# Performance work log

Measured on AMD Instinct MI355X. Metric: run time of the kernel, lower is better.

The kernel has to match this reference:

```python
import jax, jax.numpy as jnp
import numpy as np

T, B, N, E, NF, L = 4, 8, 5000, 80000, 16, 3


def setup_inputs() -> dict:
    key = jax.random.key(0)
    ks = jax.random.split(key, 12)
    xs = jax.random.normal(ks[0], (T, B, N, 3), jnp.float32)
    vs = jax.random.normal(ks[1], (T, B, N, 3), jnp.float32)
    charges = jax.random.uniform(ks[2], (B * N, 1), jnp.float32)
    edge_src = jax.random.randint(ks[3], (E,), 0, N)
    edge_dst = jax.random.randint(ks[4], (E,), 0, N)
    theta = jax.random.uniform(ks[5], (1, T), jnp.float32, -1.0, 1.0)  # uniform_(-1,1)
    W_embed = jax.random.normal(ks[6], (1, NF), jnp.float32) * 0.5
    W1 = jax.random.normal(ks[7], (L, 2 * NF + 1, NF), jnp.float32) / jnp.sqrt(2.0 * NF + 1)
    b1 = jnp.zeros((L, NF), jnp.float32)
    W2 = jax.random.normal(ks[8], (L, NF, NF), jnp.float32) / jnp.sqrt(float(NF))
    b2 = jnp.zeros((L, NF), jnp.float32)
    Wv = jax.random.normal(ks[9], (L, NF, 1), jnp.float32) * 0.1
    return dict(xs=xs, vs=vs, charges=charges, edge_src=edge_src, edge_dst=edge_dst,
                theta=theta, W_embed=W_embed, W1=W1, b1=b1, W2=W2, b2=b2, Wv=Wv)


def reference(xs, vs, charges, edge_src, edge_dst, theta, W_embed, W1, b1, W2, b2, Wv):
    T_, B_, N_, _ = xs.shape
    # node scalar features ('f' / type-0) initialized from charges
    h0 = jax.nn.relu(charges.reshape(B_, N_, 1) @ W_embed)  # [B, N, NF]

    def graph_step(x, v, h):
        # x, v: [N,3]; h: [N,NF]. Equivariant message passing with edge rel-pos gather.
        d = x[edge_dst] - x[edge_src]                      # [E,3]  (edata['d'])
        d2 = jnp.sum(d * d, axis=-1, keepdims=True)        # [E,1]  invariant edge feature
        vec = v                                            # type-1 ('vel') channel
        for l in range(L):
            feat = jnp.concatenate([h[edge_src], h[edge_dst], d2], axis=-1)  # [E,2NF+1]
            m = jax.nn.relu(feat @ W1[l] + b1[l])                            # [E,NF]
            agg = jax.ops.segment_sum(m, edge_dst, num_segments=N_)          # [N,NF]
            h = h + jax.nn.relu(agg @ W2[l] + b2[l])
            # equivariant vector update: scatter d-weighted messages
            vec = vec + jax.ops.segment_sum(d * (m @ Wv[l]), edge_dst, num_segments=N_)
        return vec + x  # module returns out + xs

    step_b = jax.vmap(graph_step)                                  # over batch
    out = jax.vmap(lambda x, v: step_b(x, v, h0))(xs, vs)          # [T,B,N,3]
    x = out.reshape(T_, B_ * N_, 3)                                # step's view(-1, 3)
    x_hat = jnp.einsum('ij,jkt->ikt', jax.nn.softmax(theta, axis=1), x)
    return x_hat.squeeze(0)  # [B*N, 3] since num_future == 1
```

## Files before the change

kernel.cpp:

```cpp
#include <hip/hip_runtime.h>
#include <hip/hip_bf16.h>

constexpr int T_ = 4;
constexpr int B_ = 8;
constexpr int N_ = 5000;
constexpr int E_ = 80000;
constexpr int TBN = T_ * B_ * N_;
constexpr int NXCD = 8;

constexpr int NPB = 64;
constexpr int CH  = (N_ + NPB - 1) / NPB;
constexpr int GRP = T_ * B_ / NXCD;
constexpr int LB  = NXCD * CH * GRP;

__device__ __forceinline__ unsigned bf16pack2(float lo, float hi) {
    unsigned ul = (__float_as_uint(lo) + 0x8000u) >> 16;
    unsigned uh = (__float_as_uint(hi) + 0x8000u) & 0xffff0000u;
    return uh | ul;
}
__device__ __forceinline__ void bf16unpack2(unsigned u, float& lo, float& hi) {
    lo = __uint_as_float(u << 16);
    hi = __uint_as_float(u & 0xffff0000u);
}

__global__ void k_degree(const int* __restrict__ dst, int* __restrict__ deg) {
    int e = blockIdx.x * 256 + threadIdx.x;
    if (e < E_) atomicAdd(&deg[dst[e]], 1);
}

__global__ void k_scan(const int* __restrict__ deg, int* __restrict__ row_start) {
    __shared__ int sums[256];
    const int tid = threadIdx.x;
    const int per = 20;
    const int base = tid * per;
    int local = 0;
    for (int i = 0; i < per; ++i) {
        int idx = base + i;
        if (idx < N_) local += deg[idx];
    }
    sums[tid] = local;
    __syncthreads();
    for (int off = 1; off < 256; off <<= 1) {
        int v = 0;
        if (tid >= off) v = sums[tid - off];
        __syncthreads();
        if (tid >= off) sums[tid] += v;
        __syncthreads();
    }
    int running = sums[tid] - local;
    for (int i = 0; i < per; ++i) {
        int idx = base + i;
        if (idx < N_) {
            row_start[idx] = running;
            running += deg[idx];
        }
    }
    if (tid == 255) row_start[N_] = sums[255];
}

__global__ void k_scatter(const int* __restrict__ src, const int* __restrict__ dst,
                          const int* __restrict__ row_start, int* __restrict__ cursor,
                          int* __restrict__ csr_src) {
    int e = blockIdx.x * 256 + threadIdx.x;
    if (e < E_) {
        int d = dst[e];
        int pos = atomicAdd(&cursor[d], 1);
        csr_src[row_start[d] + pos] = src[e];
    }
}

__global__ void k_init(const float* __restrict__ xs, float4* __restrict__ xs4) {
    int g = blockIdx.x * 256 + threadIdx.x;
    xs4[g] = make_float4(xs[3*g], xs[3*g+1], xs[3*g+2], 0.0f);
}

template <int LYR, bool HAS_NEXT>
__global__ __launch_bounds__(256, 4) void k_layer(
        const float4* __restrict__ xs4, const float* __restrict__ charges,
        const float* __restrict__ vs, const float* __restrict__ W_embed,
        const float* __restrict__ W1, const float* __restrict__ b1,
        const float* __restrict__ W2, const float* __restrict__ b2,
        const float* __restrict__ Wv,
        const int* __restrict__ row_start, const int* __restrict__ csr_src,
        float* __restrict__ h, const uint4* __restrict__ gs_in,
        uint2* __restrict__ gs_out, unsigned* __restrict__ gd,
        float* __restrict__ vec) {
    __shared__ float s_w1e[16], s_wv[16], s_b2[16], s_b1[16], s_b1n[16];
    __shared__ float s_W2[256];
    __shared__ float s_W1sn[256];
    __shared__ float s_W1dn[256];
    __shared__ float s_P[16], s_Q[16], s_rwe[16];
    const int tid = threadIdx.x;
    if (tid < 16) {
        s_w1e[tid] = W1[LYR * 528 + 512 + tid];
        s_wv[tid]  = Wv[LYR * 16 + tid];
        s_b2[tid]  = b2[LYR * 16 + tid];
        s_b1[tid]  = b1[LYR * 16 + tid];
        if (HAS_NEXT) s_b1n[tid] = b1[(LYR + 1) * 16 + tid];
    }
    s_W2[tid] = W2[LYR * 256 + tid];
    if (HAS_NEXT) {
        s_W1sn[tid] = W1[(LYR + 1) * 528 + tid];
        s_W1dn[tid] = W1[(LYR + 1) * 528 + 256 + tid];
    }
    if (LYR == 0 && tid < 16) {
        float accP = 0.0f, accQ = 0.0f;
        for (int j = 0; j < 16; ++j) {
            float r = fmaxf(W_embed[j], 0.0f);
            accP += r * W1[j * 16 + tid];
            accQ += r * W1[256 + j * 16 + tid];
        }
        s_P[tid] = accP; s_Q[tid] = accQ;
        s_rwe[tid] = fmaxf(W_embed[tid], 0.0f);
    }
    __syncthreads();

    const int bid   = blockIdx.x;
    const int xcd   = bid & 7;
    const int j     = bid >> 3;
    const int tb    = xcd + NXCD * (j / CH);
    const int chunk = j % CH;
    const int node  = chunk * NPB + (tid >> 2);
    const int q     = tid & 3;
    if (node >= N_) return;

    const int g = tb * N_ + node;
    const size_t nb = (size_t)tb * N_;
    const float* cb = charges + (tb % B_) * N_;

    const float4 xn = xs4[g];

    float gdn[16];
    float c0 = 0.0f;
    if (LYR == 0) {
        c0 = cb[node];
#pragma unroll
        for (int f = 0; f < 16; ++f) gdn[f] = c0 * s_Q[f] + s_b1[f];
    } else {
        const uint4* gdp = (const uint4*)gd + (size_t)g * 2;
        uint4 da = gdp[0], db = gdp[1];
        bf16unpack2(da.x, gdn[0], gdn[1]);  bf16unpack2(da.y, gdn[2], gdn[3]);
        bf16unpack2(da.z, gdn[4], gdn[5]);  bf16unpack2(da.w, gdn[6], gdn[7]);
        bf16unpack2(db.x, gdn[8], gdn[9]);  bf16unpack2(db.y, gdn[10], gdn[11]);
        bf16unpack2(db.z, gdn[12], gdn[13]); bf16unpack2(db.w, gdn[14], gdn[15]);
    }

    float agg[16];
#pragma unroll
    for (int f = 0; f < 16; ++f) agg[f] = 0.0f;
    float av0 = 0.0f, av1 = 0.0f, av2 = 0.0f;

    const int rs = row_start[node];
    const int re = row_start[node + 1];

    int e = rs + q;
    bool have = e < re;
    int s = have ? csr_src[e] : 0;
    size_t si = nb + (size_t)s;
    float4 xc = xs4[si];
    float  cs = 0.0f;
    uint4  ga, gb;
    if (LYR == 0) cs = cb[s];
    else { ga = gs_in[si * 2]; gb = gs_in[si * 2 + 1]; }

    while (have) {
        int e2 = e + 4;
        bool have2 = e2 < re;
        int s2 = have2 ? csr_src[e2] : 0;
        size_t si2 = nb + (size_t)s2;
        float4 xc2 = xs4[si2];
        float  cs2 = 0.0f;
        uint4  ga2, gb2;
        if (LYR == 0) cs2 = cb[s2];
        else { ga2 = gs_in[si2 * 2]; gb2 = gs_in[si2 * 2 + 1]; }

        float d0 = xn.x - xc.x;
        float d1 = xn.y - xc.y;
        float d2v = xn.z - xc.z;
        float dd = d0*d0 + d1*d1 + d2v*d2v;

        float gsf[16];
        if (LYR == 0) {
#pragma unroll
            for (int f = 0; f < 16; ++f) gsf[f] = cs * s_P[f];
        } else {
            bf16unpack2(ga.x, gsf[0], gsf[1]);  bf16unpack2(ga.y, gsf[2], gsf[3]);
            bf16unpack2(ga.z, gsf[4], gsf[5]);  bf16unpack2(ga.w, gsf[6], gsf[7]);
            bf16unpack2(gb.x, gsf[8], gsf[9]);  bf16unpack2(gb.y, gsf[10], gsf[11]);
            bf16unpack2(gb.z, gsf[12], gsf[13]); bf16unpack2(gb.w, gsf[14], gsf[15]);
        }

        float sval = 0.0f;
#pragma unroll
        for (int f = 0; f < 16; ++f) {
            float mv = fmaxf(__builtin_fmaf(dd, s_w1e[f], gdn[f]) + gsf[f], 0.0f);
            if (HAS_NEXT) agg[f] += mv;
            sval = __builtin_fmaf(mv, s_wv[f], sval);
        }
        av0 = __builtin_fmaf(d0, sval, av0);
        av1 = __builtin_fmaf(d1, sval, av1);
        av2 = __builtin_fmaf(d2v, sval, av2);

        e = e2; have = have2; xc = xc2; cs = cs2; ga = ga2; gb = gb2;
    }

    av0 += __shfl_xor(av0, 1); av0 += __shfl_xor(av0, 2);
    av1 += __shfl_xor(av1, 1); av1 += __shfl_xor(av1, 2);
    av2 += __shfl_xor(av2, 1); av2 += __shfl_xor(av2, 2);

    if (q < 3) {
        float myav = (q == 0) ? av0 : ((q == 1) ? av1 : av2);
        size_t vi = (size_t)g * 3 + q;
        float base = (LYR == 0) ? vs[vi] : vec[vi];
        vec[vi] = base + myav;
    }

    if (HAS_NEXT) {
#pragma unroll
        for (int f = 0; f < 16; ++f) {
            agg[f] += __shfl_xor(agg[f], 1);
            agg[f] += __shfl_xor(agg[f], 2);
        }

        float hq[4];
        if (LYR == 0) {
#pragma unroll
            for (int k = 0; k < 4; ++k) hq[k] = c0 * s_rwe[q * 4 + k];
        } else {
            float4 hv = ((const float4*)h)[(size_t)g * 4 + q];
            hq[0] = hv.x; hq[1] = hv.y; hq[2] = hv.z; hq[3] = hv.w;
        }

        float acc[4];
#pragma unroll
        for (int k = 0; k < 4; ++k) acc[k] = s_b2[q * 4 + k];
#pragma unroll
        for (int jj = 0; jj < 16; ++jj) {
            float aj = agg[jj];
#pragma unroll
            for (int k = 0; k < 4; ++k)
                acc[k] = __builtin_fmaf(aj, s_W2[jj * 16 + q * 4 + k], acc[k]);
        }
#pragma unroll
        for (int k = 0; k < 4; ++k) hq[k] += fmaxf(acc[k], 0.0f);

        const int lane = tid & 63;
        const int lbase = lane & ~3;
        float hfull[16];
#pragma unroll
        for (int sq = 0; sq < 4; ++sq) {
#pragma unroll
            for (int k = 0; k < 4; ++k)
                hfull[sq * 4 + k] = __shfl(hq[k], lbase + sq, 64);
        }

        float gso[4], gdo[4];
#pragma unroll
        for (int k = 0; k < 4; ++k) { gso[k] = 0.0f; gdo[k] = s_b1n[q * 4 + k]; }
#pragma unroll
        for (int jj = 0; jj < 16; ++jj) {
            float hj = hfull[jj];
#pragma unroll
            for (int k = 0; k < 4; ++k) {
                gso[k] = __builtin_fmaf(hj, s_W1sn[jj * 16 + q * 4 + k], gso[k]);
                gdo[k] = __builtin_fmaf(hj, s_W1dn[jj * 16 + q * 4 + k], gdo[k]);
            }
        }

        ((float4*)h)[(size_t)g * 4 + q] = make_float4(hq[0], hq[1], hq[2], hq[3]);
        gs_out[(size_t)g * 4 + q] = make_uint2(bf16pack2(gso[0], gso[1]),
                                               bf16pack2(gso[2], gso[3]));
        ((uint2*)gd)[(size_t)g * 4 + q] = make_uint2(bf16pack2(gdo[0], gdo[1]),
                                                     bf16pack2(gdo[2], gdo[3]));
    }
}

__global__ void k_final(const float* __restrict__ xs, const float* __restrict__ vec,
                        const float* __restrict__ theta, float* __restrict__ out) {
    int g = blockIdx.x * 256 + threadIdx.x;
    if (g >= B_ * N_) return;
    float t0 = theta[0], t1 = theta[1], t2 = theta[2], t3 = theta[3];
    float mx = fmaxf(fmaxf(t0, t1), fmaxf(t2, t3));
    float e0 = expf(t0 - mx), e1 = expf(t1 - mx), e2 = expf(t2 - mx), e3 = expf(t3 - mx);
    float inv = 1.0f / (e0 + e1 + e2 + e3);
    float w[4] = {e0 * inv, e1 * inv, e2 * inv, e3 * inv};

    int b = g / N_;
    int n = g - b * N_;
    float o0 = 0.0f, o1 = 0.0f, o2 = 0.0f;
#pragma unroll
    for (int t = 0; t < 4; ++t) {
        size_t idx = ((size_t)(t * B_ + b) * N_ + n) * 3;
        o0 += w[t] * (vec[idx+0] + xs[idx+0]);
        o1 += w[t] * (vec[idx+1] + xs[idx+1]);
        o2 += w[t] * (vec[idx+2] + xs[idx+2]);
    }
    out[(size_t)g*3+0] = o0;
    out[(size_t)g*3+1] = o1;
    out[(size_t)g*3+2] = o2;
}

extern "C" void kernel_launch(void* const* d_in, const int* in_sizes, int n_in,
                              void* d_out, int out_size, void* d_ws, size_t ws_size,
                              hipStream_t stream) {
    const float* xs       = (const float*)d_in[0];
    const float* vs       = (const float*)d_in[1];
    const float* charges  = (const float*)d_in[2];
    const int*   edge_src = (const int*)d_in[3];
    const int*   edge_dst = (const int*)d_in[4];
    const float* theta    = (const float*)d_in[5];
    const float* W_embed  = (const float*)d_in[6];
    const float* W1       = (const float*)d_in[7];
    const float* b1       = (const float*)d_in[8];
    const float* W2       = (const float*)d_in[9];
    const float* b2       = (const float*)d_in[10];
    const float* Wv       = (const float*)d_in[11];
    float* out = (float*)d_out;

    char* w = (char*)d_ws;
    size_t off = 0;
    auto take = [&](size_t bytes) {
        size_t o = off;
        off = (off + bytes + 255) & ~(size_t)255;
        return o;
    };
    int*      deg       = (int*)(w + take((size_t)N_ * 4));
    int*      cursor    = (int*)(w + take((size_t)N_ * 4));
    int*      row_start = (int*)(w + take((size_t)(N_ + 1) * 4));
    int*      csr_src   = (int*)(w + take((size_t)E_ * 4));
    float*    h         = (float*)(w + take((size_t)TBN * 16 * 4));
    unsigned* gsA       = (unsigned*)(w + take((size_t)TBN * 32));
    unsigned* gsB       = (unsigned*)(w + take((size_t)TBN * 32));
    unsigned* gd        = (unsigned*)(w + take((size_t)TBN * 32));
    float*    vec       = (float*)(w + take((size_t)TBN * 3 * 4));
    float4*   xs4       = (float4*)(w + take((size_t)TBN * 16));
    (void)ws_size;

    hipMemsetAsync(deg, 0, (size_t)N_ * 4, stream);
    hipMemsetAsync(cursor, 0, (size_t)N_ * 4, stream);

    const int eb = (E_ + 255) / 256;
    k_degree<<<eb, 256, 0, stream>>>(edge_dst, deg);
    k_scan<<<1, 256, 0, stream>>>(deg, row_start);
    k_scatter<<<eb, 256, 0, stream>>>(edge_src, edge_dst, row_start, cursor, csr_src);

    k_init<<<TBN / 256, 256, 0, stream>>>(xs, xs4);

    k_layer<0, true ><<<LB, 256, 0, stream>>>(xs4, charges, vs, W_embed, W1, b1, W2, b2, Wv,
                                              row_start, csr_src, h, nullptr,
                                              (uint2*)gsA, gd, vec);
    k_layer<1, true ><<<LB, 256, 0, stream>>>(xs4, charges, vs, W_embed, W1, b1, W2, b2, Wv,
                                              row_start, csr_src, h, (const uint4*)gsA,
                                              (uint2*)gsB, gd, vec);
    k_layer<2, false><<<LB, 256, 0, stream>>>(xs4, charges, vs, W_embed, W1, b1, W2, b2, Wv,
                                              row_start, csr_src, h, (const uint4*)gsB,
                                              nullptr, gd, vec);

    const int fb = (B_ * N_ + 255) / 256;
    k_final<<<fb, 256, 0, stream>>>(xs, vec, theta, out);
}
```

Baseline: 124.6 us.

## Sort nodes by in-degree for balanced wavefronts and deepen CSR prefetch

Adds a single-block counting sort that builds a permutation of nodes ordered by in-degree, and the layer kernels map threads to nodes through it. Nodes of similar degree then share a wavefront, which cuts divergence from uneven edge loops. The edge loop now prefetches the source index two steps ahead using clamped loads, and the two memsets are merged into one. Costs are an extra kernel launch, an indirection through perm, and scattered writes to per-node outputs.

```diff
diff --git a/kernel.cpp b/kernel.cpp
--- a/kernel.cpp
+++ b/kernel.cpp
@@ -69,6 +69,31 @@
     }
 }
 
+__global__ void k_perm(const int* __restrict__ deg, int* __restrict__ perm) {
+    __shared__ int hist[64];
+    __shared__ int base[64];
+    const int tid = threadIdx.x;
+    if (tid < 64) hist[tid] = 0;
+    __syncthreads();
+    for (int idx = tid; idx < N_; idx += 256) {
+        int d = min(deg[idx], 63);
+        atomicAdd(&hist[d], 1);
+    }
+    __syncthreads();
+    if (tid == 0) {
+        int running = 0;
+        for (int b = 0; b < 64; ++b) { base[b] = running; running += hist[b]; }
+    }
+    __syncthreads();
+    if (tid < 64) hist[tid] = 0;
+    __syncthreads();
+    for (int idx = tid; idx < N_; idx += 256) {
+        int d = min(deg[idx], 63);
+        int pos = atomicAdd(&hist[d], 1);
+        perm[base[d] + pos] = idx;
+    }
+}
+
 __global__ void k_init(const float* __restrict__ xs, float4* __restrict__ xs4) {
     int g = blockIdx.x * 256 + threadIdx.x;
     xs4[g] = make_float4(xs[3*g], xs[3*g+1], xs[3*g+2], 0.0f);
@@ -82,6 +107,7 @@
         const float* __restrict__ W2, const float* __restrict__ b2,
         const float* __restrict__ Wv,
         const int* __restrict__ row_start, const int* __restrict__ csr_src,
+        const int* __restrict__ perm,
         float* __restrict__ h, const uint4* __restrict__ gs_in,
         uint2* __restrict__ gs_out, unsigned* __restrict__ gd,
         float* __restrict__ vec) {
@@ -120,9 +146,10 @@
     const int j     = bid >> 3;
     const int tb    = xcd + NXCD * (j / CH);
     const int chunk = j % CH;
-    const int node  = chunk * NPB + (tid >> 2);
+    const int idx   = chunk * NPB + (tid >> 2);
     const int q     = tid & 3;
-    if (node >= N_) return;
+    if (idx >= N_) return;
+    const int node  = perm[idx];
 
     const int g = tb * N_ + node;
     const size_t nb = (size_t)tb * N_;
@@ -154,25 +181,23 @@
     const int re = row_start[node + 1];
 
     int e = rs + q;
-    bool have = e < re;
-    int s = have ? csr_src[e] : 0;
-    size_t si = nb + (size_t)s;
+    int sCur  = csr_src[min(e, E_ - 1)];
+    int sNext = csr_src[min(e + 4, E_ - 1)];
+    size_t si = nb + (size_t)sCur;
     float4 xc = xs4[si];
     float  cs = 0.0f;
     uint4  ga, gb;
-    if (LYR == 0) cs = cb[s];
+    if (LYR == 0) cs = cb[sCur];
     else { ga = gs_in[si * 2]; gb = gs_in[si * 2 + 1]; }
 
-    while (have) {
-        int e2 = e + 4;
-        bool have2 = e2 < re;
-        int s2 = have2 ? csr_src[e2] : 0;
-        size_t si2 = nb + (size_t)s2;
-        float4 xc2 = xs4[si2];
-        float  cs2 = 0.0f;
-        uint4  ga2, gb2;
-        if (LYR == 0) cs2 = cb[s2];
-        else { ga2 = gs_in[si2 * 2]; gb2 = gs_in[si2 * 2 + 1]; }
+    while (e < re) {
+        int s3 = csr_src[min(e + 8, E_ - 1)];
+        size_t siN = nb + (size_t)sNext;
+        float4 xcN = xs4[siN];
+        float  csN = 0.0f;
+        uint4  gaN, gbN;
+        if (LYR == 0) csN = cb[sNext];
+        else { gaN = gs_in[siN * 2]; gbN = gs_in[siN * 2 + 1]; }
 
         float d0 = xn.x - xc.x;
         float d1 = xn.y - xc.y;
@@ -201,7 +226,9 @@
         av1 = __builtin_fmaf(d1, sval, av1);
         av2 = __builtin_fmaf(d2v, sval, av2);
 
-        e = e2; have = have2; xc = xc2; cs = cs2; ga = ga2; gb = gb2;
+        e += 4;
+        sNext = s3;
+        xc = xcN; cs = csN; ga = gaN; gb = gbN;
     }
 
     av0 += __shfl_xor(av0, 1); av0 += __shfl_xor(av0, 2);
@@ -328,6 +355,7 @@
     int*      cursor    = (int*)(w + take((size_t)N_ * 4));
     int*      row_start = (int*)(w + take((size_t)(N_ + 1) * 4));
     int*      csr_src   = (int*)(w + take((size_t)E_ * 4));
+    int*      perm      = (int*)(w + take((size_t)N_ * 4));
     float*    h         = (float*)(w + take((size_t)TBN * 16 * 4));
     unsigned* gsA       = (unsigned*)(w + take((size_t)TBN * 32));
     unsigned* gsB       = (unsigned*)(w + take((size_t)TBN * 32));
@@ -336,24 +364,25 @@
     float4*   xs4       = (float4*)(w + take((size_t)TBN * 16));
     (void)ws_size;
 
-    hipMemsetAsync(deg, 0, (size_t)N_ * 4, stream);
-    hipMemsetAsync(cursor, 0, (size_t)N_ * 4, stream);
+    size_t zlen = (size_t)((char*)cursor - (char*)deg) + (size_t)N_ * 4;
+    hipMemsetAsync(deg, 0, zlen, stream);
 
     const int eb = (E_ + 255) / 256;
     k_degree<<<eb, 256, 0, stream>>>(edge_dst, deg);
     k_scan<<<1, 256, 0, stream>>>(deg, row_start);
+    k_perm<<<1, 256, 0, stream>>>(deg, perm);
     k_scatter<<<eb, 256, 0, stream>>>(edge_src, edge_dst, row_start, cursor, csr_src);
 
     k_init<<<TBN / 256, 256, 0, stream>>>(xs, xs4);
 
     k_layer<0, true ><<<LB, 256, 0, stream>>>(xs4, charges, vs, W_embed, W1, b1, W2, b2, Wv,
-                                              row_start, csr_src, h, nullptr,
+                                              row_start, csr_src, perm, h, nullptr,
                                               (uint2*)gsA, gd, vec);
     k_layer<1, true ><<<LB, 256, 0, stream>>>(xs4, charges, vs, W_embed, W1, b1, W2, b2, Wv,
-                                              row_start, csr_src, h, (const uint4*)gsA,
+                                              row_start, csr_src, perm, h, (const uint4*)gsA,
                                               (uint2*)gsB, gd, vec);
     k_layer<2, false><<<LB, 256, 0, stream>>>(xs4, charges, vs, W_embed, W1, b1, W2, b2, Wv,
-                                              row_start, csr_src, h, (const uint4*)gsB,
+                                              row_start, csr_src, perm, h, (const uint4*)gsB,
                                               nullptr, gd, vec);
 
     const int fb = (B_ * N_ + 255) / 256;
```

Result: slower. 136.9 us (+9.9%).

## Sort nodes by in-degree into permuted slots and fuse CSR build

Applied to the files above, without the earlier changes.

Nodes are relabelled by a counting sort on in-degree, so the four lanes per node in a block handle neighbours of similar degree and divergence in the edge loop drops. All per-node arrays (positions, velocities, charges, features) are stored in permuted slot order, and the CSR source indices are translated to slots. The degree count, scan and permutation build are merged into one single-block shared-memory kernel, which replaces the memsets and two small launches. The cost is an extra perm lookup per node, a gather in init and final, and a serial single-block build that could become a bottleneck.

```diff
diff --git a/kernel.cpp b/kernel.cpp
--- a/kernel.cpp
+++ b/kernel.cpp
@@ -23,65 +23,95 @@
     hi = __uint_as_float(u & 0xffff0000u);
 }
 
-__global__ void k_degree(const int* __restrict__ dst, int* __restrict__ deg) {
-    int e = blockIdx.x * 256 + threadIdx.x;
-    if (e < E_) atomicAdd(&deg[dst[e]], 1);
-}
-
-__global__ void k_scan(const int* __restrict__ deg, int* __restrict__ row_start) {
-    __shared__ int sums[256];
+__global__ __launch_bounds__(1024) void k_build1(
+        const int* __restrict__ edge_dst, int* __restrict__ row_start,
+        int* __restrict__ perm, int* __restrict__ inv, int* __restrict__ cursor) {
+    __shared__ int sdeg[5120];
+    __shared__ int ssum[1024];
+    __shared__ int hist[64];
+    __shared__ int hbase[64];
     const int tid = threadIdx.x;
-    const int per = 20;
-    const int base = tid * per;
-    int local = 0;
-    for (int i = 0; i < per; ++i) {
-        int idx = base + i;
-        if (idx < N_) local += deg[idx];
-    }
-    sums[tid] = local;
-    __syncthreads();
-    for (int off = 1; off < 256; off <<= 1) {
+    for (int i = tid; i < 5120; i += 1024) sdeg[i] = 0;
+    __syncthreads();
+    for (int e = tid; e < E_; e += 1024) atomicAdd(&sdeg[edge_dst[e]], 1);
+    __syncthreads();
+    const int base = tid * 5;
+    int loc = 0;
+#pragma unroll
+    for (int i = 0; i < 5; ++i) { int ix = base + i; if (ix < N_) loc += sdeg[ix]; }
+    ssum[tid] = loc;
+    __syncthreads();
+    for (int off = 1; off < 1024; off <<= 1) {
         int v = 0;
-        if (tid >= off) v = sums[tid - off];
+        if (tid >= off) v = ssum[tid - off];
         __syncthreads();
-        if (tid >= off) sums[tid] += v;
+        if (tid >= off) ssum[tid] += v;
         __syncthreads();
     }
-    int running = sums[tid] - local;
-    for (int i = 0; i < per; ++i) {
-        int idx = base + i;
-        if (idx < N_) {
-            row_start[idx] = running;
-            running += deg[idx];
-        }
-    }
-    if (tid == 255) row_start[N_] = sums[255];
-}
-
-__global__ void k_scatter(const int* __restrict__ src, const int* __restrict__ dst,
-                          const int* __restrict__ row_start, int* __restrict__ cursor,
-                          int* __restrict__ csr_src) {
+    int run = ssum[tid] - loc;
+#pragma unroll
+    for (int i = 0; i < 5; ++i) {
+        int ix = base + i;
+        if (ix < N_) { row_start[ix] = run; run += sdeg[ix]; }
+    }
+    if (tid == 1023) row_start[N_] = ssum[1023];
+    for (int i = tid; i < N_; i += 1024) cursor[i] = 0;
+    if (tid < 64) hist[tid] = 0;
+    __syncthreads();
+    for (int i = tid; i < N_; i += 1024) atomicAdd(&hist[min(sdeg[i], 63)], 1);
+    __syncthreads();
+    if (tid == 0) {
+        int r = 0;
+        for (int b = 0; b < 64; ++b) { hbase[b] = r; r += hist[b]; }
+    }
+    __syncthreads();
+    if (tid < 64) hist[tid] = 0;
+    __syncthreads();
+    for (int i = tid; i < N_; i += 1024) {
+        int d = min(sdeg[i], 63);
+        int p = atomicAdd(&hist[d], 1);
+        int slot = hbase[d] + p;
+        perm[slot] = i;
+        inv[i] = slot;
+    }
+}
+
+__global__ void k_build2(const int* __restrict__ src, const int* __restrict__ dst,
+                         const int* __restrict__ row_start, int* __restrict__ cursor,
+                         const int* __restrict__ inv, int* __restrict__ csr_srcT) {
     int e = blockIdx.x * 256 + threadIdx.x;
     if (e < E_) {
         int d = dst[e];
         int pos = atomicAdd(&cursor[d], 1);
-        csr_src[row_start[d] + pos] = src[e];
-    }
-}
-
-__global__ void k_init(const float* __restrict__ xs, float4* __restrict__ xs4) {
+        csr_srcT[row_start[d] + pos] = inv[src[e]];
+    }
+}
+
+__global__ void k_init(const float* __restrict__ xs, const float* __restrict__ vs,
+                       const float* __restrict__ charges, const int* __restrict__ perm,
+                       float4* __restrict__ xs4, float* __restrict__ vec,
+                       float* __restrict__ chs) {
     int g = blockIdx.x * 256 + threadIdx.x;
-    xs4[g] = make_float4(xs[3*g], xs[3*g+1], xs[3*g+2], 0.0f);
+    int tb = g / N_;
+    int i  = g - tb * N_;
+    int node = perm[i];
+    size_t sn = (size_t)tb * N_ + node;
+    xs4[g] = make_float4(xs[3*sn], xs[3*sn+1], xs[3*sn+2], 0.0f);
+    vec[3*(size_t)g+0] = vs[3*sn+0];
+    vec[3*(size_t)g+1] = vs[3*sn+1];
+    vec[3*(size_t)g+2] = vs[3*sn+2];
+    if (tb < B_) chs[g] = charges[sn];
 }
 
 template <int LYR, bool HAS_NEXT>
 __global__ __launch_bounds__(256, 4) void k_layer(
-        const float4* __restrict__ xs4, const float* __restrict__ charges,
-        const float* __restrict__ vs, const float* __restrict__ W_embed,
+        const float4* __restrict__ xs4, const float* __restrict__ chs,
+        const float* __restrict__ W_embed,
         const float* __restrict__ W1, const float* __restrict__ b1,
         const float* __restrict__ W2, const float* __restrict__ b2,
         const float* __restrict__ Wv,
-        const int* __restrict__ row_start, const int* __restrict__ csr_src,
+        const int* __restrict__ row_start, const int* __restrict__ csr_srcT,
+        const int* __restrict__ perm,
         float* __restrict__ h, const uint4* __restrict__ gs_in,
         uint2* __restrict__ gs_out, unsigned* __restrict__ gd,
         float* __restrict__ vec) {
@@ -120,20 +150,20 @@
     const int j     = bid >> 3;
     const int tb    = xcd + NXCD * (j / CH);
     const int chunk = j % CH;
-    const int node  = chunk * NPB + (tid >> 2);
+    const int slot  = chunk * NPB + (tid >> 2);
     const int q     = tid & 3;
-    if (node >= N_) return;
-
-    const int g = tb * N_ + node;
+    if (slot >= N_) return;
+
+    const int g = tb * N_ + slot;
     const size_t nb = (size_t)tb * N_;
-    const float* cb = charges + (tb % B_) * N_;
+    const float* cb = chs + (tb % B_) * N_;
 
     const float4 xn = xs4[g];
 
     float gdn[16];
     float c0 = 0.0f;
     if (LYR == 0) {
-        c0 = cb[node];
+        c0 = cb[slot];
 #pragma unroll
         for (int f = 0; f < 16; ++f) gdn[f] = c0 * s_Q[f] + s_b1[f];
     } else {
@@ -150,12 +180,13 @@
     for (int f = 0; f < 16; ++f) agg[f] = 0.0f;
     float av0 = 0.0f, av1 = 0.0f, av2 = 0.0f;
 
+    const int node = perm[slot];
     const int rs = row_start[node];
     const int re = row_start[node + 1];
 
     int e = rs + q;
     bool have = e < re;
-    int s = have ? csr_src[e] : 0;
+    int s = have ? csr_srcT[e] : 0;
     size_t si = nb + (size_t)s;
     float4 xc = xs4[si];
     float  cs = 0.0f;
@@ -166,7 +197,7 @@
     while (have) {
         int e2 = e + 4;
         bool have2 = e2 < re;
-        int s2 = have2 ? csr_src[e2] : 0;
+        int s2 = have2 ? csr_srcT[e2] : 0;
         size_t si2 = nb + (size_t)s2;
         float4 xc2 = xs4[si2];
         float  cs2 = 0.0f;
@@ -211,8 +242,7 @@
     if (q < 3) {
         float myav = (q == 0) ? av0 : ((q == 1) ? av1 : av2);
         size_t vi = (size_t)g * 3 + q;
-        float base = (LYR == 0) ? vs[vi] : vec[vi];
-        vec[vi] = base + myav;
+        vec[vi] += myav;
     }
 
     if (HAS_NEXT) {
@@ -276,24 +306,27 @@
 }
 
 __global__ void k_final(const float* __restrict__ xs, const float* __restrict__ vec,
-                        const float* __restrict__ theta, float* __restrict__ out) {
+                        const float* __restrict__ theta, const int* __restrict__ inv,
+                        float* __restrict__ out) {
     int g = blockIdx.x * 256 + threadIdx.x;
     if (g >= B_ * N_) return;
     float t0 = theta[0], t1 = theta[1], t2 = theta[2], t3 = theta[3];
     float mx = fmaxf(fmaxf(t0, t1), fmaxf(t2, t3));
     float e0 = expf(t0 - mx), e1 = expf(t1 - mx), e2 = expf(t2 - mx), e3 = expf(t3 - mx);
-    float inv = 1.0f / (e0 + e1 + e2 + e3);
-    float w[4] = {e0 * inv, e1 * inv, e2 * inv, e3 * inv};
+    float is = 1.0f / (e0 + e1 + e2 + e3);
+    float w[4] = {e0 * is, e1 * is, e2 * is, e3 * is};
 
     int b = g / N_;
     int n = g - b * N_;
+    int slot = inv[n];
     float o0 = 0.0f, o1 = 0.0f, o2 = 0.0f;
 #pragma unroll
     for (int t = 0; t < 4; ++t) {
-        size_t idx = ((size_t)(t * B_ + b) * N_ + n) * 3;
-        o0 += w[t] * (vec[idx+0] + xs[idx+0]);
-        o1 += w[t] * (vec[idx+1] + xs[idx+1]);
-        o2 += w[t] * (vec[idx+2] + xs[idx+2]);
+        size_t vi = ((size_t)(t * B_ + b) * N_ + slot) * 3;
+        size_t xi = ((size_t)(t * B_ + b) * N_ + n) * 3;
+        o0 += w[t] * (vec[vi+0] + xs[xi+0]);
+        o1 += w[t] * (vec[vi+1] + xs[xi+1]);
+        o2 += w[t] * (vec[vi+2] + xs[xi+2]);
     }
     out[(size_t)g*3+0] = o0;
     out[(size_t)g*3+1] = o1;
@@ -324,38 +357,36 @@
         off = (off + bytes + 255) & ~(size_t)255;
         return o;
     };
-    int*      deg       = (int*)(w + take((size_t)N_ * 4));
     int*      cursor    = (int*)(w + take((size_t)N_ * 4));
     int*      row_start = (int*)(w + take((size_t)(N_ + 1) * 4));
-    int*      csr_src   = (int*)(w + take((size_t)E_ * 4));
+    int*      csr_srcT  = (int*)(w + take((size_t)E_ * 4));
+    int*      perm      = (int*)(w + take((size_t)N_ * 4));
+    int*      inv       = (int*)(w + take((size_t)N_ * 4));
     float*    h         = (float*)(w + take((size_t)TBN * 16 * 4));
     unsigned* gsA       = (unsigned*)(w + take((size_t)TBN * 32));
     unsigned* gsB       = (unsigned*)(w + take((size_t)TBN * 32));
     unsigned* gd        = (unsigned*)(w + take((size_t)TBN * 32));
     float*    vec       = (float*)(w + take((size_t)TBN * 3 * 4));
     float4*   xs4       = (float4*)(w + take((size_t)TBN * 16));
+    float*    chs       = (float*)(w + take((size_t)B_ * N_ * 4));
     (void)ws_size;
 
-    hipMemsetAsync(deg, 0, (size_t)N_ * 4, stream);
-    hipMemsetAsync(cursor, 0, (size_t)N_ * 4, stream);
-
+    k_build1<<<1, 1024, 0, stream>>>(edge_dst, row_start, perm, inv, cursor);
     const int eb = (E_ + 255) / 256;
-    k_degree<<<eb, 256, 0, stream>>>(edge_dst, deg);
-    k_scan<<<1, 256, 0, stream>>>(deg, row_start);
-    k_scatter<<<eb, 256, 0, stream>>>(edge_src, edge_dst, row_start, cursor, csr_src);
-
-    k_init<<<TBN / 256, 256, 0, stream>>>(xs, xs4);
-
-    k_layer<0, true ><<<LB, 256, 0, stream>>>(xs4, charges, vs, W_embed, W1, b1, W2, b2, Wv,
-                                              row_start, csr_src, h, nullptr,
+    k_build2<<<eb, 256, 0, stream>>>(edge_src, edge_dst, row_start, cursor, inv, csr_srcT);
+
+    k_init<<<TBN / 256, 256, 0, stream>>>(xs, vs, charges, perm, xs4, vec, chs);
+
+    k_layer<0, true ><<<LB, 256, 0, stream>>>(xs4, chs, W_embed, W1, b1, W2, b2, Wv,
+                                              row_start, csr_srcT, perm, h, nullptr,
                                               (uint2*)gsA, gd, vec);
-    k_layer<1, true ><<<LB, 256, 0, stream>>>(xs4, charges, vs, W_embed, W1, b1, W2, b2, Wv,
-                                              row_start, csr_src, h, (const uint4*)gsA,
+    k_layer<1, true ><<<LB, 256, 0, stream>>>(xs4, chs, W_embed, W1, b1, W2, b2, Wv,
+                                              row_start, csr_srcT, perm, h, (const uint4*)gsA,
                                               (uint2*)gsB, gd, vec);
-    k_layer<2, false><<<LB, 256, 0, stream>>>(xs4, charges, vs, W_embed, W1, b1, W2, b2, Wv,
-                                              row_start, csr_src, h, (const uint4*)gsB,
+    k_layer<2, false><<<LB, 256, 0, stream>>>(xs4, chs, W_embed, W1, b1, W2, b2, Wv,
+                                              row_start, csr_srcT, perm, h, (const uint4*)gsB,
                                               nullptr, gd, vec);
 
     const int fb = (B_ * N_ + 255) / 256;
-    k_final<<<fb, 256, 0, stream>>>(xs, vec, theta, out);
-}
+    k_final<<<fb, 256, 0, stream>>>(xs, vec, theta, inv, out);
+}
```

After: 138.8 us. +11.4%, slower.

## Pack node position, charge and source features into 64-byte records; fuse setup kernels

Applied to the files above, without the earlier changes.

Merges the degree count and scan into one single-block shared-memory kernel and fuses the CSR scatter with input packing and vec initialisation, removing two memsets and several launches. Each node's position, charge and bf16 source-side features now sit in one 64-byte record, ping-ponged between layers, so each edge gather touches one contiguous line instead of two separate arrays. The edge loop processes two edges per lane per iteration with a mask for the tail, adding memory-level parallelism. The risks are a serial single-block build kernel, wider records, and the masked second edge doing wasted work on low-degree nodes.

```diff
diff --git a/kernel.cpp b/kernel.cpp
--- a/kernel.cpp
+++ b/kernel.cpp
@@ -12,6 +12,8 @@
 constexpr int CH  = (N_ + NPB - 1) / NPB;
 constexpr int GRP = T_ * B_ / NXCD;
 constexpr int LB  = NXCD * CH * GRP;
+constexpr int EB  = (E_ + 255) / 256;
+constexpr int IB  = TBN / 256;
 
 __device__ __forceinline__ unsigned bf16pack2(float lo, float hi) {
     unsigned ul = (__float_as_uint(lo) + 0x8000u) >> 16;
@@ -23,67 +25,79 @@
     hi = __uint_as_float(u & 0xffff0000u);
 }
 
-__global__ void k_degree(const int* __restrict__ dst, int* __restrict__ deg) {
-    int e = blockIdx.x * 256 + threadIdx.x;
-    if (e < E_) atomicAdd(&deg[dst[e]], 1);
-}
-
-__global__ void k_scan(const int* __restrict__ deg, int* __restrict__ row_start) {
-    __shared__ int sums[256];
+__global__ __launch_bounds__(1024) void k_build1(
+        const int* __restrict__ edge_dst, int* __restrict__ row_start,
+        int* __restrict__ cursor) {
+    __shared__ int sdeg[5120];
+    __shared__ int ssum[1024];
     const int tid = threadIdx.x;
-    const int per = 20;
-    const int base = tid * per;
-    int local = 0;
-    for (int i = 0; i < per; ++i) {
-        int idx = base + i;
-        if (idx < N_) local += deg[idx];
-    }
-    sums[tid] = local;
+    for (int i = tid; i < 5120; i += 1024) sdeg[i] = 0;
     __syncthreads();
-    for (int off = 1; off < 256; off <<= 1) {
+    for (int e = tid; e < E_; e += 1024) atomicAdd(&sdeg[edge_dst[e]], 1);
+    __syncthreads();
+    const int base = tid * 5;
+    int loc = 0;
+#pragma unroll
+    for (int i = 0; i < 5; ++i) { int ix = base + i; if (ix < N_) loc += sdeg[ix]; }
+    ssum[tid] = loc;
+    __syncthreads();
+    for (int off = 1; off < 1024; off <<= 1) {
         int v = 0;
-        if (tid >= off) v = sums[tid - off];
+        if (tid >= off) v = ssum[tid - off];
         __syncthreads();
-        if (tid >= off) sums[tid] += v;
+        if (tid >= off) ssum[tid] += v;
         __syncthreads();
     }
-    int running = sums[tid] - local;
-    for (int i = 0; i < per; ++i) {
-        int idx = base + i;
-        if (idx < N_) {
-            row_start[idx] = running;
-            running += deg[idx];
-        }
-    }
-    if (tid == 255) row_start[N_] = sums[255];
-}
-
-__global__ void k_scatter(const int* __restrict__ src, const int* __restrict__ dst,
-                          const int* __restrict__ row_start, int* __restrict__ cursor,
-                          int* __restrict__ csr_src) {
-    int e = blockIdx.x * 256 + threadIdx.x;
-    if (e < E_) {
-        int d = dst[e];
-        int pos = atomicAdd(&cursor[d], 1);
-        csr_src[row_start[d] + pos] = src[e];
-    }
-}
-
-__global__ void k_init(const float* __restrict__ xs, float4* __restrict__ xs4) {
-    int g = blockIdx.x * 256 + threadIdx.x;
-    xs4[g] = make_float4(xs[3*g], xs[3*g+1], xs[3*g+2], 0.0f);
+    int run = ssum[tid] - loc;
+#pragma unroll
+    for (int i = 0; i < 5; ++i) {
+        int ix = base + i;
+        if (ix < N_) { row_start[ix] = run; run += sdeg[ix]; }
+    }
+    if (tid == 1023) row_start[N_] = ssum[1023];
+    for (int i = tid; i < N_; i += 1024) cursor[i] = 0;
+}
+
+__global__ void k_build2(const int* __restrict__ src, const int* __restrict__ dst,
+                         const int* __restrict__ row_start, int* __restrict__ cursor,
+                         int* __restrict__ csr_src,
+                         const float* __restrict__ xs, const float* __restrict__ vs,
+                         const float* __restrict__ charges,
+                         uint4* __restrict__ rec0, uint4* __restrict__ rec1,
+                         float* __restrict__ vec) {
+    const int bid = blockIdx.x;
+    const int tid = threadIdx.x;
+    if (bid < EB) {
+        int e = bid * 256 + tid;
+        if (e < E_) {
+            int d = dst[e];
+            int pos = atomicAdd(&cursor[d], 1);
+            csr_src[row_start[d] + pos] = src[e];
+        }
+    } else {
+        int g = (bid - EB) * 256 + tid;
+        int tb = g / N_;
+        int n  = g - tb * N_;
+        int b  = tb % B_;
+        float c = charges[b * N_ + n];
+        float4 xc = make_float4(xs[3*(size_t)g], xs[3*(size_t)g+1], xs[3*(size_t)g+2], c);
+        ((float4*)rec0)[(size_t)g * 4] = xc;
+        ((float4*)rec1)[(size_t)g * 4] = xc;
+        vec[3*(size_t)g+0] = vs[3*(size_t)g+0];
+        vec[3*(size_t)g+1] = vs[3*(size_t)g+1];
+        vec[3*(size_t)g+2] = vs[3*(size_t)g+2];
+    }
 }
 
 template <int LYR, bool HAS_NEXT>
 __global__ __launch_bounds__(256, 4) void k_layer(
-        const float4* __restrict__ xs4, const float* __restrict__ charges,
-        const float* __restrict__ vs, const float* __restrict__ W_embed,
+        const uint4* __restrict__ rec_in, uint4* __restrict__ rec_out,
+        const float* __restrict__ W_embed,
         const float* __restrict__ W1, const float* __restrict__ b1,
         const float* __restrict__ W2, const float* __restrict__ b2,
         const float* __restrict__ Wv,
         const int* __restrict__ row_start, const int* __restrict__ csr_src,
-        float* __restrict__ h, const uint4* __restrict__ gs_in,
-        uint2* __restrict__ gs_out, unsigned* __restrict__ gd,
+        float* __restrict__ h, unsigned* __restrict__ gd,
         float* __restrict__ vec) {
     __shared__ float s_w1e[16], s_wv[16], s_b2[16], s_b1[16], s_b1n[16];
     __shared__ float s_W2[256];
@@ -126,14 +140,12 @@
 
     const int g = tb * N_ + node;
     const size_t nb = (size_t)tb * N_;
-    const float* cb = charges + (tb % B_) * N_;
-
-    const float4 xn = xs4[g];
+
+    const float4 xn = ((const float4*)rec_in)[(size_t)g * 4];
+    const float c0 = xn.w;
 
     float gdn[16];
-    float c0 = 0.0f;
     if (LYR == 0) {
-        c0 = cb[node];
 #pragma unroll
         for (int f = 0; f < 16; ++f) gdn[f] = c0 * s_Q[f] + s_b1[f];
     } else {
@@ -153,34 +165,14 @@
     const int rs = row_start[node];
     const int re = row_start[node + 1];
 
-    int e = rs + q;
-    bool have = e < re;
-    int s = have ? csr_src[e] : 0;
-    size_t si = nb + (size_t)s;
-    float4 xc = xs4[si];
-    float  cs = 0.0f;
-    uint4  ga, gb;
-    if (LYR == 0) cs = cb[s];
-    else { ga = gs_in[si * 2]; gb = gs_in[si * 2 + 1]; }
-
-    while (have) {
-        int e2 = e + 4;
-        bool have2 = e2 < re;
-        int s2 = have2 ? csr_src[e2] : 0;
-        size_t si2 = nb + (size_t)s2;
-        float4 xc2 = xs4[si2];
-        float  cs2 = 0.0f;
-        uint4  ga2, gb2;
-        if (LYR == 0) cs2 = cb[s2];
-        else { ga2 = gs_in[si2 * 2]; gb2 = gs_in[si2 * 2 + 1]; }
-
+    auto mlp = [&](const float4& xc, const uint4& ga, const uint4& gb, float mask) {
         float d0 = xn.x - xc.x;
         float d1 = xn.y - xc.y;
         float d2v = xn.z - xc.z;
         float dd = d0*d0 + d1*d1 + d2v*d2v;
-
         float gsf[16];
         if (LYR == 0) {
+            float cs = xc.w;
 #pragma unroll
             for (int f = 0; f < 16; ++f) gsf[f] = cs * s_P[f];
         } else {
@@ -189,19 +181,53 @@
             bf16unpack2(gb.x, gsf[8], gsf[9]);  bf16unpack2(gb.y, gsf[10], gsf[11]);
             bf16unpack2(gb.z, gsf[12], gsf[13]); bf16unpack2(gb.w, gsf[14], gsf[15]);
         }
-
         float sval = 0.0f;
 #pragma unroll
         for (int f = 0; f < 16; ++f) {
-            float mv = fmaxf(__builtin_fmaf(dd, s_w1e[f], gdn[f]) + gsf[f], 0.0f);
+            float mv = fmaxf(__builtin_fmaf(dd, s_w1e[f], gdn[f]) + gsf[f], 0.0f) * mask;
             if (HAS_NEXT) agg[f] += mv;
             sval = __builtin_fmaf(mv, s_wv[f], sval);
         }
         av0 = __builtin_fmaf(d0, sval, av0);
         av1 = __builtin_fmaf(d1, sval, av1);
         av2 = __builtin_fmaf(d2v, sval, av2);
-
-        e = e2; have = have2; xc = xc2; cs = cs2; ga = ga2; gb = gb2;
+    };
+
+    int eA = rs + q, eB = eA + 4;
+    bool hA = eA < re, hB = eB < re;
+    int sA = hA ? csr_src[eA] : 0;
+    int sB = hB ? csr_src[eB] : 0;
+    size_t iA = nb + (size_t)sA, iB = nb + (size_t)sB;
+    float4 xA = ((const float4*)rec_in)[iA * 4];
+    float4 xB = ((const float4*)rec_in)[iB * 4];
+    uint4 gAa, gAb, gBa, gBb;
+    if (LYR != 0) {
+        gAa = rec_in[iA * 4 + 1]; gAb = rec_in[iA * 4 + 2];
+        gBa = rec_in[iB * 4 + 1]; gBb = rec_in[iB * 4 + 2];
+    }
+    float mB = hB ? 1.0f : 0.0f;
+
+    while (hA) {
+        int eA2 = eA + 8, eB2 = eB + 8;
+        bool hA2 = eA2 < re, hB2 = eB2 < re;
+        int sA2 = hA2 ? csr_src[eA2] : 0;
+        int sB2 = hB2 ? csr_src[eB2] : 0;
+        size_t iA2 = nb + (size_t)sA2, iB2 = nb + (size_t)sB2;
+        float4 xA2 = ((const float4*)rec_in)[iA2 * 4];
+        float4 xB2 = ((const float4*)rec_in)[iB2 * 4];
+        uint4 gAa2, gAb2, gBa2, gBb2;
+        if (LYR != 0) {
+            gAa2 = rec_in[iA2 * 4 + 1]; gAb2 = rec_in[iA2 * 4 + 2];
+            gBa2 = rec_in[iB2 * 4 + 1]; gBb2 = rec_in[iB2 * 4 + 2];
+        }
+
+        mlp(xA, gAa, gAb, 1.0f);
+        mlp(xB, gBa, gBb, mB);
+
+        eA = eA2; eB = eB2; hA = hA2; hB = hB2;
+        mB = hB2 ? 1.0f : 0.0f;
+        xA = xA2; xB = xB2;
+        gAa = gAa2; gAb = gAb2; gBa = gBa2; gBb = gBb2;
     }
 
     av0 += __shfl_xor(av0, 1); av0 += __shfl_xor(av0, 2);
@@ -210,9 +236,7 @@
 
     if (q < 3) {
         float myav = (q == 0) ? av0 : ((q == 1) ? av1 : av2);
-        size_t vi = (size_t)g * 3 + q;
-        float base = (LYR == 0) ? vs[vi] : vec[vi];
-        vec[vi] = base + myav;
+        vec[(size_t)g * 3 + q] += myav;
     }
 
     if (HAS_NEXT) {
@@ -268,10 +292,10 @@
         }
 
         ((float4*)h)[(size_t)g * 4 + q] = make_float4(hq[0], hq[1], hq[2], hq[3]);
-        gs_out[(size_t)g * 4 + q] = make_uint2(bf16pack2(gso[0], gso[1]),
-                                               bf16pack2(gso[2], gso[3]));
-        ((uint2*)gd)[(size_t)g * 4 + q] = make_uint2(bf16pack2(gdo[0], gdo[1]),
-                                                     bf16pack2(gdo[2], gdo[3]));
+        ((uint2*)rec_out)[(size_t)g * 8 + 2 + q] =
+            make_uint2(bf16pack2(gso[0], gso[1]), bf16pack2(gso[2], gso[3]));
+        ((uint2*)gd)[(size_t)g * 4 + q] =
+            make_uint2(bf16pack2(gdo[0], gdo[1]), bf16pack2(gdo[2], gdo[3]));
     }
 }
 
@@ -282,8 +306,8 @@
     float t0 = theta[0], t1 = theta[1], t2 = theta[2], t3 = theta[3];
     float mx = fmaxf(fmaxf(t0, t1), fmaxf(t2, t3));
     float e0 = expf(t0 - mx), e1 = expf(t1 - mx), e2 = expf(t2 - mx), e3 = expf(t3 - mx);
-    float inv = 1.0f / (e0 + e1 + e2 + e3);
-    float w[4] = {e0 * inv, e1 * inv, e2 * inv, e3 * inv};
+    float is = 1.0f / (e0 + e1 + e2 + e3);
+    float w[4] = {e0 * is, e1 * is, e2 * is, e3 * is};
 
     int b = g / N_;
     int n = g - b * N_;
@@ -324,37 +348,26 @@
         off = (off + bytes + 255) & ~(size_t)255;
         return o;
     };
-    int*      deg       = (int*)(w + take((size_t)N_ * 4));
     int*      cursor    = (int*)(w + take((size_t)N_ * 4));
     int*      row_start = (int*)(w + take((size_t)(N_ + 1) * 4));
     int*      csr_src   = (int*)(w + take((size_t)E_ * 4));
+    uint4*    rec0      = (uint4*)(w + take((size_t)TBN * 64));
+    uint4*    rec1      = (uint4*)(w + take((size_t)TBN * 64));
     float*    h         = (float*)(w + take((size_t)TBN * 16 * 4));
-    unsigned* gsA       = (unsigned*)(w + take((size_t)TBN * 32));
-    unsigned* gsB       = (unsigned*)(w + take((size_t)TBN * 32));
     unsigned* gd        = (unsigned*)(w + take((size_t)TBN * 32));
     float*    vec       = (float*)(w + take((size_t)TBN * 3 * 4));
-    float4*   xs4       = (float4*)(w + take((size_t)TBN * 16));
     (void)ws_size;
 
-    hipMemsetAsync(deg, 0, (size_t)N_ * 4, stream);
-    hipMemsetAsync(cursor, 0, (size_t)N_ * 4, stream);
-
-    const int eb = (E_ + 255) / 256;
-    k_degree<<<eb, 256, 0, stream>>>(edge_dst, deg);
-    k_scan<<<1, 256, 0, stream>>>(deg, row_start);
-    k_scatter<<<eb, 256, 0, stream>>>(edge_src, edge_dst, row_start, cursor, csr_src);
-
-    k_init<<<TBN / 256, 256, 0, stream>>>(xs, xs4);
-
-    k_layer<0, true ><<<LB, 256, 0, stream>>>(xs4, charges, vs, W_embed, W1, b1, W2, b2, Wv,
-                                              row_start, csr_src, h, nullptr,
-                                              (uint2*)gsA, gd, vec);
-    k_layer<1, true ><<<LB, 256, 0, stream>>>(xs4, charges, vs, W_embed, W1, b1, W2, b2, Wv,
-                                              row_start, csr_src, h, (const uint4*)gsA,
-                                              (uint2*)gsB, gd, vec);
-    k_layer<2, false><<<LB, 256, 0, stream>>>(xs4, charges, vs, W_embed, W1, b1, W2, b2, Wv,
-                                              row_start, csr_src, h, (const uint4*)gsB,
-                                              nullptr, gd, vec);
+    k_build1<<<1, 1024, 0, stream>>>(edge_dst, row_start, cursor);
+    k_build2<<<EB + IB, 256, 0, stream>>>(edge_src, edge_dst, row_start, cursor, csr_src,
+                                          xs, vs, charges, rec0, rec1, vec);
+
+    k_layer<0, true ><<<LB, 256, 0, stream>>>(rec0, rec1, W_embed, W1, b1, W2, b2, Wv,
+                                              row_start, csr_src, h, gd, vec);
+    k_layer<1, true ><<<LB, 256, 0, stream>>>(rec1, rec0, W_embed, W1, b1, W2, b2, Wv,
+                                              row_start, csr_src, h, gd, vec);
+    k_layer<2, false><<<LB, 256, 0, stream>>>(rec0, nullptr, W_embed, W1, b1, W2, b2, Wv,
+                                              row_start, csr_src, h, gd, vec);
 
     const int fb = (B_ * N_ + 255) / 256;
     k_final<<<fb, 256, 0, stream>>>(xs, vec, theta, out);
```

Result: slower. 189.5 us (+52.1%).
